# Kernel tuning notes

Hardware: AMD Instinct MI355X
Metric: run time of the kernel (lower is better)

## Reference

```python
import jax, jax.numpy as jnp
import numpy as np

TEMPERATURE = 0.1
EPS = 1e-12  # F.normalize eps


def setup_inputs() -> dict:
    key = jax.random.key(0)
    k1, k2 = jax.random.split(key)
    B, D = 4096, 128
    return {
        "x_i": jax.random.normal(k1, (B, D), dtype=jnp.float32),
        "x_j": jax.random.normal(k2, (B, D), dtype=jnp.float32),
    }


def _l2_normalize(x):
    n = jnp.sqrt(jnp.sum(x * x, axis=1, keepdims=True))
    return x / jnp.maximum(n, EPS)


def reference(x_i, x_j):
    B = x_i.shape[0]
    z = jnp.concatenate([_l2_normalize(x_i), _l2_normalize(x_j)], axis=0)  # [2B, D]
    # cosine similarity of unit-norm rows == dot product -> single GEMM
    sim = z @ z.T  # [2B, 2B]
    idx = jnp.arange(B)
    sim_ij = sim[idx, idx + B]   # diag(sim, +B)
    sim_ji = sim[idx + B, idx]   # diag(sim, -B)
    positives = jnp.concatenate([sim_ij, sim_ji], axis=0)  # [2B]
    neg_mask = 1.0 - jnp.eye(2 * B, dtype=sim.dtype)
    denominator = jnp.sum(neg_mask * jnp.exp(sim / TEMPERATURE), axis=1)  # [2B]
    # -log(exp(pos/t) / denom) = -(pos/t - log denom)
    loss_partial = jnp.log(denominator) - positives / TEMPERATURE
    return jnp.sum(loss_partial) / (2 * B)
```

## Files before the change

### kernel.cpp

```cpp
#include <hip/hip_runtime.h>
#include <stdint.h>

#define D_DIM 128
#define NROW 8192
#define L2EPS 1e-12f
#define SCALE_PRE 0.9495707f
#define LN2 0.6931471805599453f
#define NPART 50

typedef __attribute__((ext_vector_type(4))) int   i32x4;
typedef __attribute__((ext_vector_type(8))) int   i32x8;
typedef __attribute__((ext_vector_type(4))) float f32x4;

#define AS1 __attribute__((address_space(1)))
#define AS3 __attribute__((address_space(3)))

static __device__ inline void gload_lds16(const void* g, void* l) {
    __builtin_amdgcn_global_load_lds((const AS1 uint32_t*)g, (AS3 uint32_t*)l, 16, 0, 0);
}

static __device__ inline i32x8 cat8(i32x4 lo, i32x4 hi) {
    i32x8 r;
    r[0] = lo[0]; r[1] = lo[1]; r[2] = lo[2]; r[3] = lo[3];
    r[4] = hi[0]; r[5] = hi[1]; r[6] = hi[2]; r[7] = hi[3];
    return r;
}

static __device__ __forceinline__ float fexp2(float x) {
#if __has_builtin(__builtin_amdgcn_exp2f)
    return __builtin_amdgcn_exp2f(x);
#else
    float r;
    asm("v_exp_f32 %0, %1" : "=v"(r) : "v"(x));
    return r;
#endif
}

static __device__ __forceinline__ float dpp_row_sum16(float v) {
    union { float f; int i; } u, s;
    u.f = v;
    s.i = __builtin_amdgcn_update_dpp(0, u.i, 0x118, 0xF, 0xF, true); u.f += s.f;
    s.i = __builtin_amdgcn_update_dpp(0, u.i, 0x114, 0xF, 0xF, true); u.f += s.f;
    s.i = __builtin_amdgcn_update_dpp(0, u.i, 0x112, 0xF, 0xF, true); u.f += s.f;
    s.i = __builtin_amdgcn_update_dpp(0, u.i, 0x111, 0xF, 0xF, true); u.f += s.f;
    return u.f;
}

__global__ __launch_bounds__(256) void k_normalize(
        const float* __restrict__ xi, const float* __restrict__ xj,
        uint8_t* __restrict__ z8, float* __restrict__ pos_acc,
        float* __restrict__ logsum, unsigned* __restrict__ done_ct) {
    const int wave = threadIdx.x >> 6;
    const int lane = threadIdx.x & 63;
    const int row = blockIdx.x * 4 + wave;
    const float* src = (row < 4096) ? (xi + (size_t)row * D_DIM)
                                    : (xj + (size_t)(row - 4096) * D_DIM);
    float2 v = *(const float2*)(src + lane * 2);
    float ss = v.x * v.x + v.y * v.y;
#pragma unroll
    for (int m = 32; m >= 1; m >>= 1) ss += __shfl_xor(ss, m, 64);
    const float scale = SCALE_PRE / fmaxf(sqrtf(ss), L2EPS);
    const int pk = __builtin_amdgcn_cvt_pk_fp8_f32(v.x * scale, v.y * scale, 0, false);
    *(ushort*)(z8 + (size_t)row * D_DIM + lane * 2) = (ushort)pk;

    if (blockIdx.x == 0 && threadIdx.x == 0) {
        pos_acc[0] = 0.0f; logsum[0] = 0.0f; done_ct[0] = 0u;
    }
}

__global__ __launch_bounds__(256) void k_gemm(
        const uint8_t* __restrict__ z8, float* __restrict__ part,
        float* __restrict__ pos_acc) {
    __shared__ __align__(16) uint8_t lds[32768];

    const int t = threadIdx.x;
    const int wave = t >> 6, lane = t & 63;
    const int quad = lane >> 4, lc = lane & 15;

    const int mb = blockIdx.x >> 6;
    const int rb = blockIdx.x & 63;
    const int rowbase = rb * 128;
    const bool diag = (mb == 16);
    const int c1 = diag ? rb : (rb + 2 * mb + 1) & 63;
    const int c2 = (rb + 2 * mb + 2) & 63;

    {
        const uint8_t* zb1 = z8 + (size_t)c1 * 128 * D_DIM;
#pragma unroll
        for (int q = 0; q < 4; q++) {
            const int s = q * 256 + t;
            const int r = s >> 3;
            const int g = (s & 7) ^ (r & 7);
            gload_lds16(zb1 + (size_t)r * D_DIM + g * 16, &lds[s * 16]);
        }
        if (!diag) {
            const uint8_t* zb2 = z8 + (size_t)c2 * 128 * D_DIM;
#pragma unroll
            for (int q = 0; q < 4; q++) {
                const int s = q * 256 + t;
                const int r = s >> 3;
                const int g = (s & 7) ^ (r & 7);
                gload_lds16(zb2 + (size_t)r * D_DIM + g * 16, &lds[16384 + s * 16]);
            }
        }
    }

    i32x8 afr[2];
    {
        const uint8_t* pa = z8 + (size_t)(rowbase + wave * 32 + lc) * D_DIM + quad * 32;
#pragma unroll
        for (int i = 0; i < 2; i++) {
            i32x4 lo = *(const i32x4*)(pa + i * 16 * D_DIM);
            i32x4 hi = *(const i32x4*)(pa + i * 16 * D_DIM + 16);
            afr[i] = cat8(lo, hi);
        }
    }

    asm volatile("s_waitcnt vmcnt(0)" ::: "memory");
    __syncthreads();

    float rs[2][4] = {{0.f,0.f,0.f,0.f},{0.f,0.f,0.f,0.f}};
    float cs[16];
#pragma unroll
    for (int j = 0; j < 16; j++) cs[j] = 0.f;
    float posp = 0.f;
    const int rl0 = wave * 32 + quad * 4;

#define MFMA_J(j, A0, A1)                                                     \
    i32x4 blo, bhi; {                                                         \
        const int rowb = ((j) * 16 + lc) * D_DIM;                             \
        blo = *(const i32x4*)&lds[rowb + (((quad * 2)     ^ (lc & 7)) * 16)]; \
        bhi = *(const i32x4*)&lds[rowb + (((quad * 2 + 1) ^ (lc & 7)) * 16)]; \
    }                                                                         \
    const i32x8 bfr = cat8(blo, bhi);                                         \
    f32x4 z4 = {0.f, 0.f, 0.f, 0.f};                                          \
    f32x4 A0 = __builtin_amdgcn_mfma_scale_f32_16x16x128_f8f6f4(              \
                   afr[0], bfr, z4, 0, 0, 0, 131, 0, 127);                    \
    f32x4 A1 = __builtin_amdgcn_mfma_scale_f32_16x16x128_f8f6f4(              \
                   afr[1], bfr, z4, 0, 0, 0, 131, 0, 127);

    if (!diag) {
#pragma unroll
        for (int j = 0; j < 8; j++) {
            MFMA_J(j, a0, a1)
#pragma unroll
            for (int r = 0; r < 4; r++) {
                const float e0 = fexp2(a0[r]);
                const float e1 = fexp2(a1[r]);
                rs[0][r] += e0;
                rs[1][r] += e1;
                cs[j] += e0 + e1;
            }
        }
        if (mb < 15) {
#pragma unroll
            for (int j = 8; j < 16; j++) {
                MFMA_J(j, a0, a1)
#pragma unroll
                for (int r = 0; r < 4; r++) {
                    const float e0 = fexp2(a0[r]);
                    const float e1 = fexp2(a1[r]);
                    rs[0][r] += e0;
                    rs[1][r] += e1;
                    cs[j] += e0 + e1;
                }
            }
        } else {
#pragma unroll
            for (int j = 8; j < 16; j++) {
                MFMA_J(j, a0, a1)
                const int clb = (j - 8) * 16 + lc;
#pragma unroll
                for (int i = 0; i < 2; i++)
#pragma unroll
                    for (int r = 0; r < 4; r++) {
                        const float s = (i ? a1 : a0)[r];
                        const float e = 0.5f * fexp2(s);
                        if (clb == rl0 + i * 16 + r) posp += s;
                        rs[i][r] += e;
                        cs[j] += e;
                    }
            }
        }
    } else {
#pragma unroll
        for (int j = 0; j < 8; j++) {
            MFMA_J(j, a0, a1)
            const int cl = j * 16 + lc;
#pragma unroll
            for (int i = 0; i < 2; i++)
#pragma unroll
                for (int r = 0; r < 4; r++) {
                    const float s = (i ? a1 : a0)[r];
                    const float e = (cl > rl0 + i * 16 + r) ? fexp2(s) : 0.f;
                    rs[i][r] += e;
                    cs[j] += e;
                }
        }
    }
#undef MFMA_J

#pragma unroll
    for (int i = 0; i < 2; i++)
#pragma unroll
        for (int r = 0; r < 4; r++) {
            const float v = dpp_row_sum16(rs[i][r]);
            if (lc == 15)
                part[(size_t)mb * NROW + rowbase + rl0 + i * 16 + r] = v;
        }

#pragma unroll
    for (int j = 0; j < 16; j++) {
        cs[j] += __shfl_xor(cs[j], 16, 64);
        cs[j] += __shfl_xor(cs[j], 32, 64);
    }
    __syncthreads();
    float* colred = (float*)lds;
    if (quad == 0) {
#pragma unroll
        for (int j = 0; j < 16; j++)
            colred[wave * 256 + j * 16 + lc] = cs[j];
    }
    __syncthreads();
    if (t < 256) {
        const float v = colred[t] + colred[256 + t] + colred[512 + t] + colred[768 + t];
        if (!diag) {
            const int slot = 17 + 2 * mb + (t >> 7);
            const int band = (t < 128) ? c1 : c2;
            part[(size_t)slot * NROW + band * 128 + (t & 127)] = v;
        } else if (t < 128) {
            part[(size_t)49 * NROW + c1 * 128 + t] = v;
        }
    }

    if (mb == 15) {
#pragma unroll
        for (int mm = 32; mm >= 1; mm >>= 1) posp += __shfl_xor(posp, mm, 64);
        if (lane == 0) atomicAdd(pos_acc, posp);
    }
}

__global__ __launch_bounds__(256) void k_logsum(
        const float* __restrict__ part, float* __restrict__ pos_acc,
        float* __restrict__ logsum, unsigned* __restrict__ done_ct,
        float* __restrict__ out) {
    const int row = blockIdx.x * 256 + threadIdx.x;
    float d = 0.f;
#pragma unroll
    for (int p = 0; p < NPART; p++) d += part[(size_t)p * NROW + row];
    float v = __logf(d);
#pragma unroll
    for (int m = 32; m >= 1; m >>= 1) v += __shfl_xor(v, m, 64);
    if ((threadIdx.x & 63) == 0) atomicAdd(logsum, v);
    __threadfence();
    __syncthreads();
    if (threadIdx.x == 0) {
        const unsigned prev = atomicAdd(done_ct, 1u);
        if (prev == gridDim.x - 1) {
            __threadfence();
            const float ls = atomicAdd(logsum, 0.0f);
            const float pp = atomicAdd(pos_acc, 0.0f);
            out[0] = (ls - pp * LN2) / (float)NROW;
        }
    }
}

extern "C" void kernel_launch(void* const* d_in, const int* in_sizes, int n_in,
                              void* d_out, int out_size, void* d_ws, size_t ws_size,
                              hipStream_t stream) {
    const float* xi = (const float*)d_in[0];
    const float* xj = (const float*)d_in[1];
    uint8_t* z8 = (uint8_t*)d_ws;
    float* part = (float*)(z8 + (size_t)NROW * D_DIM);
    float* pos_acc = part + (size_t)NPART * NROW;
    float* logsum = pos_acc + 1;
    unsigned* done_ct = (unsigned*)(logsum + 1);
    float* out = (float*)d_out;

    hipLaunchKernelGGL(k_normalize, dim3(NROW / 4), dim3(256), 0, stream,
                       xi, xj, z8, pos_acc, logsum, done_ct);
    hipLaunchKernelGGL(k_gemm, dim3(17 * 64), dim3(256), 0, stream,
                       z8, part, pos_acc);
    hipLaunchKernelGGL(k_logsum, dim3(NROW / 256), dim3(256), 0, stream,
                       part, pos_acc, logsum, done_ct, out);
}
```

Measured before the change: 80.46 us.

## Fuse logsum reduction into GEMM kernel via last-blocks tail with atomic counter

Removes the separate k_logsum launch. The last 32 GEMM blocks to finish instead spin-wait until every block has completed, then each reduces 256 rows of partial sums, takes the log and accumulates it. A second counter picks the final block that writes the scalar output. This saves a kernel launch and its gap, but adds spin-waiting that depends on all blocks making forward progress, and the tail work now runs serially after the GEMM.

```diff
diff --git a/kernel.cpp b/kernel.cpp
--- a/kernel.cpp
+++ b/kernel.cpp
@@ -7,6 +7,8 @@
 #define SCALE_PRE 0.9495707f
 #define LN2 0.6931471805599453f
 #define NPART 50
+#define GRID (17 * 64)
+#define NTAIL 32
 
 typedef __attribute__((ext_vector_type(4))) int   i32x4;
 typedef __attribute__((ext_vector_type(8))) int   i32x8;
@@ -49,7 +51,7 @@
 __global__ __launch_bounds__(256) void k_normalize(
         const float* __restrict__ xi, const float* __restrict__ xj,
         uint8_t* __restrict__ z8, float* __restrict__ pos_acc,
-        float* __restrict__ logsum, unsigned* __restrict__ done_ct) {
+        float* __restrict__ logsum, unsigned* __restrict__ ctrs) {
     const int wave = threadIdx.x >> 6;
     const int lane = threadIdx.x & 63;
     const int row = blockIdx.x * 4 + wave;
@@ -64,13 +66,16 @@
     *(ushort*)(z8 + (size_t)row * D_DIM + lane * 2) = (ushort)pk;
 
     if (blockIdx.x == 0 && threadIdx.x == 0) {
-        pos_acc[0] = 0.0f; logsum[0] = 0.0f; done_ct[0] = 0u;
+        pos_acc[0] = 0.0f; logsum[0] = 0.0f;
+        ctrs[0] = 0u;
+        ctrs[1] = 0u;
     }
 }
 
 __global__ __launch_bounds__(256) void k_gemm(
         const uint8_t* __restrict__ z8, float* __restrict__ part,
-        float* __restrict__ pos_acc) {
+        float* __restrict__ pos_acc, float* __restrict__ logsum,
+        unsigned* __restrict__ ctrs, float* __restrict__ out) {
     __shared__ __align__(16) uint8_t lds[32768];
 
     const int t = threadIdx.x;
@@ -238,29 +243,39 @@
         for (int mm = 32; mm >= 1; mm >>= 1) posp += __shfl_xor(posp, mm, 64);
         if (lane == 0) atomicAdd(pos_acc, posp);
     }
-}
-
-__global__ __launch_bounds__(256) void k_logsum(
-        const float* __restrict__ part, float* __restrict__ pos_acc,
-        float* __restrict__ logsum, unsigned* __restrict__ done_ct,
-        float* __restrict__ out) {
-    const int row = blockIdx.x * 256 + threadIdx.x;
-    float d = 0.f;
-#pragma unroll
-    for (int p = 0; p < NPART; p++) d += part[(size_t)p * NROW + row];
-    float v = __logf(d);
-#pragma unroll
-    for (int m = 32; m >= 1; m >>= 1) v += __shfl_xor(v, m, 64);
-    if ((threadIdx.x & 63) == 0) atomicAdd(logsum, v);
-    __threadfence();
-    __syncthreads();
-    if (threadIdx.x == 0) {
-        const unsigned prev = atomicAdd(done_ct, 1u);
-        if (prev == gridDim.x - 1) {
-            __threadfence();
-            const float ls = atomicAdd(logsum, 0.0f);
-            const float pp = atomicAdd(pos_acc, 0.0f);
-            out[0] = (ls - pp * LN2) / (float)NROW;
+
+    __syncthreads();
+    if (t == 0) {
+        __threadfence();
+        ((volatile unsigned*)lds)[0] = atomicAdd(ctrs, 1u);
+    }
+    __syncthreads();
+    const unsigned prev = ((volatile unsigned*)lds)[0];
+    if (prev >= (unsigned)(GRID - NTAIL)) {
+        if (t == 0) {
+            while (__hip_atomic_load(ctrs, __ATOMIC_RELAXED,
+                                     __HIP_MEMORY_SCOPE_AGENT) < (unsigned)GRID)
+                __builtin_amdgcn_s_sleep(2);
+        }
+        __syncthreads();
+        __threadfence();
+        const int row = (int)(prev - (unsigned)(GRID - NTAIL)) * 256 + t;
+        float d = 0.f;
+#pragma unroll
+        for (int p = 0; p < NPART; p++) d += part[(size_t)p * NROW + row];
+        float v = __logf(d);
+#pragma unroll
+        for (int m = 32; m >= 1; m >>= 1) v += __shfl_xor(v, m, 64);
+        if ((t & 63) == 0) atomicAdd(logsum, v);
+        __threadfence();
+        __syncthreads();
+        if (t == 0) {
+            const unsigned p2 = atomicAdd(ctrs + 1, 1u);
+            if (p2 == (unsigned)(NTAIL - 1)) {
+                const float ls = atomicAdd(logsum, 0.0f);
+                const float pp = atomicAdd(pos_acc, 0.0f);
+                out[0] = (ls - pp * LN2) / (float)NROW;
+            }
         }
     }
 }
@@ -274,13 +289,11 @@
     float* part = (float*)(z8 + (size_t)NROW * D_DIM);
     float* pos_acc = part + (size_t)NPART * NROW;
     float* logsum = pos_acc + 1;
-    unsigned* done_ct = (unsigned*)(logsum + 1);
+    unsigned* ctrs = (unsigned*)(logsum + 1);
     float* out = (float*)d_out;
 
     hipLaunchKernelGGL(k_normalize, dim3(NROW / 4), dim3(256), 0, stream,
-                       xi, xj, z8, pos_acc, logsum, done_ct);
-    hipLaunchKernelGGL(k_gemm, dim3(17 * 64), dim3(256), 0, stream,
-                       z8, part, pos_acc);
-    hipLaunchKernelGGL(k_logsum, dim3(NROW / 256), dim3(256), 0, stream,
-                       part, pos_acc, logsum, done_ct, out);
-}
+                       xi, xj, z8, pos_acc, logsum, ctrs);
+    hipLaunchKernelGGL(k_gemm, dim3(GRID), dim3(256), 0, stream,
+                       z8, part, pos_acc, logsum, ctrs, out);
+}
```

Result: slower. 112.0 us (+39.2%).

## Load B operands directly from global memory instead of staging through LDS

Applied to the files above, without the earlier changes.

Removes the global-to-LDS staging of the two 128-row column bands. Each wave now reads its B fragments straight from global memory (L2/cache) per MFMA step. The LDS footprint shrinks to a 4 KB column-reduction buffer and launch bounds request 4 blocks per CU, which removes the initial barrier and raises occupancy. The cost is that every wave redundantly fetches the same B data through the vector memory path with uncoalesced 32-byte reads, and the memory latency is no longer hidden behind one bulk load.

```diff
diff --git a/kernel.cpp b/kernel.cpp
--- a/kernel.cpp
+++ b/kernel.cpp
@@ -11,13 +11,6 @@
 typedef __attribute__((ext_vector_type(4))) int   i32x4;
 typedef __attribute__((ext_vector_type(8))) int   i32x8;
 typedef __attribute__((ext_vector_type(4))) float f32x4;
-
-#define AS1 __attribute__((address_space(1)))
-#define AS3 __attribute__((address_space(3)))
-
-static __device__ inline void gload_lds16(const void* g, void* l) {
-    __builtin_amdgcn_global_load_lds((const AS1 uint32_t*)g, (AS3 uint32_t*)l, 16, 0, 0);
-}
 
 static __device__ inline i32x8 cat8(i32x4 lo, i32x4 hi) {
     i32x8 r;
@@ -68,10 +61,10 @@
     }
 }
 
-__global__ __launch_bounds__(256) void k_gemm(
+__global__ __launch_bounds__(256, 4) void k_gemm(
         const uint8_t* __restrict__ z8, float* __restrict__ part,
         float* __restrict__ pos_acc) {
-    __shared__ __align__(16) uint8_t lds[32768];
+    __shared__ float colred[1024];
 
     const int t = threadIdx.x;
     const int wave = t >> 6, lane = t & 63;
@@ -84,26 +77,10 @@
     const int c1 = diag ? rb : (rb + 2 * mb + 1) & 63;
     const int c2 = (rb + 2 * mb + 2) & 63;
 
-    {
-        const uint8_t* zb1 = z8 + (size_t)c1 * 128 * D_DIM;
-#pragma unroll
-        for (int q = 0; q < 4; q++) {
-            const int s = q * 256 + t;
-            const int r = s >> 3;
-            const int g = (s & 7) ^ (r & 7);
-            gload_lds16(zb1 + (size_t)r * D_DIM + g * 16, &lds[s * 16]);
-        }
-        if (!diag) {
-            const uint8_t* zb2 = z8 + (size_t)c2 * 128 * D_DIM;
-#pragma unroll
-            for (int q = 0; q < 4; q++) {
-                const int s = q * 256 + t;
-                const int r = s >> 3;
-                const int g = (s & 7) ^ (r & 7);
-                gload_lds16(zb2 + (size_t)r * D_DIM + g * 16, &lds[16384 + s * 16]);
-            }
-        }
-    }
+    const uint8_t* zb1 = z8 + (size_t)c1 * 128 * D_DIM;
+    const uint8_t* zb2 = z8 + (size_t)c2 * 128 * D_DIM;
+    const size_t boff = (size_t)lc * D_DIM + quad * 32;
+    const uint8_t* bband[2] = { zb1 + boff, (diag ? zb1 : zb2) + boff };
 
     i32x8 afr[2];
     {
@@ -116,9 +93,6 @@
         }
     }
 
-    asm volatile("s_waitcnt vmcnt(0)" ::: "memory");
-    __syncthreads();
-
     float rs[2][4] = {{0.f,0.f,0.f,0.f},{0.f,0.f,0.f,0.f}};
     float cs[16];
 #pragma unroll
@@ -128,9 +102,9 @@
 
 #define MFMA_J(j, A0, A1)                                                     \
     i32x4 blo, bhi; {                                                         \
-        const int rowb = ((j) * 16 + lc) * D_DIM;                             \
-        blo = *(const i32x4*)&lds[rowb + (((quad * 2)     ^ (lc & 7)) * 16)]; \
-        bhi = *(const i32x4*)&lds[rowb + (((quad * 2 + 1) ^ (lc & 7)) * 16)]; \
+        const uint8_t* pb = bband[(j) >> 3] + (size_t)(((j) & 7) * 16) * D_DIM; \
+        blo = *(const i32x4*)pb;                                              \
+        bhi = *(const i32x4*)(pb + 16);                                       \
     }                                                                         \
     const i32x8 bfr = cat8(blo, bhi);                                         \
     f32x4 z4 = {0.f, 0.f, 0.f, 0.f};                                          \
@@ -214,8 +188,6 @@
         cs[j] += __shfl_xor(cs[j], 16, 64);
         cs[j] += __shfl_xor(cs[j], 32, 64);
     }
-    __syncthreads();
-    float* colred = (float*)lds;
     if (quad == 0) {
 #pragma unroll
         for (int j = 0; j < 16; j++)
```

New measurement: 91.49 us. 13.7% more time.

## Enlarge off-diagonal GEMM tiles to 512x256 per block and split diagonal blocks

Applied to the files above, without the earlier changes.

Off-diagonal work is regrouped so each block computes four 128-row bands against two 128-column bands. Each wave holds a full 128-row A fragment set in registers, and five column bands (80KB) are staged in LDS. This cuts the block count from 1088 to 320 and raises operand reuse per LDS load. Diagonal blocks become a separate simplified path. The costs are much higher register and LDS pressure, lower occupancy, and fewer blocks for load balancing across CUs.

```diff
diff --git a/kernel.cpp b/kernel.cpp
--- a/kernel.cpp
+++ b/kernel.cpp
@@ -68,24 +68,153 @@
     }
 }
 
-__global__ __launch_bounds__(256) void k_gemm(
+__global__ __launch_bounds__(256, 2) void k_gemm(
         const uint8_t* __restrict__ z8, float* __restrict__ part,
         float* __restrict__ pos_acc) {
-    __shared__ __align__(16) uint8_t lds[32768];
+    __shared__ __align__(16) uint8_t lds[81920];
 
     const int t = threadIdx.x;
     const int wave = t >> 6, lane = t & 63;
     const int quad = lane >> 4, lc = lane & 15;
-
-    const int mb = blockIdx.x >> 6;
-    const int rb = blockIdx.x & 63;
+    const int bid = blockIdx.x;
+
+    if (bid < 256) {
+        const int mb = bid >> 4;
+        const int rb4 = bid & 15;
+        const int base = 4 * rb4 + 2 * mb + 1;
+
+#pragma unroll
+        for (int q = 0; q < 20; q++) {
+            const int s = q * 256 + t;
+            const int bl = s >> 10;
+            const int r = (s >> 3) & 127;
+            const int g = (s & 7) ^ (r & 7);
+            const int gb = (base + bl) & 63;
+            gload_lds16(z8 + (size_t)gb * 128 * D_DIM + (size_t)r * D_DIM + g * 16,
+                        &lds[s * 16]);
+        }
+
+        const int arow0 = (4 * rb4 + wave) * 128;
+        i32x8 afr[8];
+        {
+            const uint8_t* pa = z8 + (size_t)(arow0 + lc) * D_DIM + quad * 32;
+#pragma unroll
+            for (int i = 0; i < 8; i++) {
+                i32x4 lo = *(const i32x4*)(pa + (size_t)i * 16 * D_DIM);
+                i32x4 hi = *(const i32x4*)(pa + (size_t)i * 16 * D_DIM + 16);
+                afr[i] = cat8(lo, hi);
+            }
+        }
+
+        asm volatile("s_waitcnt vmcnt(0)" ::: "memory");
+        __syncthreads();
+
+        float rs[8][4];
+#pragma unroll
+        for (int i = 0; i < 8; i++)
+#pragma unroll
+            for (int r = 0; r < 4; r++) rs[i][r] = 0.f;
+        float cs[16];
+#pragma unroll
+        for (int j = 0; j < 16; j++) cs[j] = 0.f;
+        float posp = 0.f;
+
+#define HB_FRAG(j)                                                            \
+        i32x4 blo, bhi; {                                                     \
+            const int rowb = (wave + ((j) >> 3)) * 16384 +                    \
+                             (((j) & 7) * 16 + lc) * 128;                     \
+            blo = *(const i32x4*)&lds[rowb + (((quad * 2)     ^ (lc & 7)) * 16)]; \
+            bhi = *(const i32x4*)&lds[rowb + (((quad * 2 + 1) ^ (lc & 7)) * 16)]; \
+        }                                                                     \
+        const i32x8 bfr = cat8(blo, bhi);                                     \
+        f32x4 acc[8];                                                         \
+        {                                                                     \
+            const f32x4 z4 = {0.f, 0.f, 0.f, 0.f};                            \
+            _Pragma("unroll")                                                 \
+            for (int i = 0; i < 8; i++)                                       \
+                acc[i] = __builtin_amdgcn_mfma_scale_f32_16x16x128_f8f6f4(    \
+                             afr[i], bfr, z4, 0, 0, 0, 131, 0, 127);          \
+        }
+
+#pragma unroll
+        for (int j = 0; j < 8; j++) {
+            HB_FRAG(j)
+#pragma unroll
+            for (int i = 0; i < 8; i++)
+#pragma unroll
+                for (int r = 0; r < 4; r++) {
+                    const float e = fexp2(acc[i][r]);
+                    rs[i][r] += e;
+                    cs[j] += e;
+                }
+        }
+        if (mb < 15) {
+#pragma unroll
+            for (int j = 8; j < 16; j++) {
+                HB_FRAG(j)
+#pragma unroll
+                for (int i = 0; i < 8; i++)
+#pragma unroll
+                    for (int r = 0; r < 4; r++) {
+                        const float e = fexp2(acc[i][r]);
+                        rs[i][r] += e;
+                        cs[j] += e;
+                    }
+            }
+        } else {
+#pragma unroll
+            for (int j = 8; j < 16; j++) {
+                HB_FRAG(j)
+#pragma unroll
+                for (int i = 0; i < 8; i++)
+#pragma unroll
+                    for (int r = 0; r < 4; r++) {
+                        const float s = acc[i][r];
+                        const float e = 0.5f * fexp2(s);
+                        if (((j & 7) == i) && (lc == quad * 4 + r)) posp += s;
+                        rs[i][r] += e;
+                        cs[j] += e;
+                    }
+            }
+        }
+#undef HB_FRAG
+
+#pragma unroll
+        for (int i = 0; i < 8; i++)
+#pragma unroll
+            for (int r = 0; r < 4; r++) {
+                const float v = dpp_row_sum16(rs[i][r]);
+                if (lc == 15)
+                    part[(size_t)mb * NROW + arow0 + i * 16 + quad * 4 + r] = v;
+            }
+
+#pragma unroll
+        for (int j = 0; j < 16; j++) {
+            cs[j] += __shfl_xor(cs[j], 16, 64);
+            cs[j] += __shfl_xor(cs[j], 32, 64);
+        }
+        if (quad == 0) {
+#pragma unroll
+            for (int j = 0; j < 16; j++) {
+                const int gb = (base + wave + (j >> 3)) & 63;
+                const int slot = 17 + 2 * mb + (j >> 3);
+                part[(size_t)slot * NROW + gb * 128 + (j & 7) * 16 + lc] = cs[j];
+            }
+        }
+
+        if (mb == 15) {
+#pragma unroll
+            for (int mm = 32; mm >= 1; mm >>= 1) posp += __shfl_xor(posp, mm, 64);
+            if (lane == 0) atomicAdd(pos_acc, posp);
+        }
+        return;
+    }
+
+    const int rb = bid - 256;
     const int rowbase = rb * 128;
-    const bool diag = (mb == 16);
-    const int c1 = diag ? rb : (rb + 2 * mb + 1) & 63;
-    const int c2 = (rb + 2 * mb + 2) & 63;
 
     {
-        const uint8_t* zb1 = z8 + (size_t)c1 * 128 * D_DIM;
+        const uint8_t* zb1 = z8 + (size_t)rb * 128 * D_DIM;
 #pragma unroll
         for (int q = 0; q < 4; q++) {
             const int s = q * 256 + t;
@@ -93,16 +222,6 @@
             const int g = (s & 7) ^ (r & 7);
             gload_lds16(zb1 + (size_t)r * D_DIM + g * 16, &lds[s * 16]);
         }
-        if (!diag) {
-            const uint8_t* zb2 = z8 + (size_t)c2 * 128 * D_DIM;
-#pragma unroll
-            for (int q = 0; q < 4; q++) {
-                const int s = q * 256 + t;
-                const int r = s >> 3;
-                const int g = (s & 7) ^ (r & 7);
-                gload_lds16(zb2 + (size_t)r * D_DIM + g * 16, &lds[16384 + s * 16]);
-            }
-        }
     }
 
     i32x8 afr[2];
@@ -123,82 +242,32 @@
     float cs[16];
 #pragma unroll
     for (int j = 0; j < 16; j++) cs[j] = 0.f;
-    float posp = 0.f;
     const int rl0 = wave * 32 + quad * 4;
 
-#define MFMA_J(j, A0, A1)                                                     \
-    i32x4 blo, bhi; {                                                         \
-        const int rowb = ((j) * 16 + lc) * D_DIM;                             \
-        blo = *(const i32x4*)&lds[rowb + (((quad * 2)     ^ (lc & 7)) * 16)]; \
-        bhi = *(const i32x4*)&lds[rowb + (((quad * 2 + 1) ^ (lc & 7)) * 16)]; \
-    }                                                                         \
-    const i32x8 bfr = cat8(blo, bhi);                                         \
-    f32x4 z4 = {0.f, 0.f, 0.f, 0.f};                                          \
-    f32x4 A0 = __builtin_amdgcn_mfma_scale_f32_16x16x128_f8f6f4(              \
-                   afr[0], bfr, z4, 0, 0, 0, 131, 0, 127);                    \
-    f32x4 A1 = __builtin_amdgcn_mfma_scale_f32_16x16x128_f8f6f4(              \
-                   afr[1], bfr, z4, 0, 0, 0, 131, 0, 127);
-
-    if (!diag) {
-#pragma unroll
-        for (int j = 0; j < 8; j++) {
-            MFMA_J(j, a0, a1)
+#pragma unroll
+    for (int j = 0; j < 8; j++) {
+        i32x4 blo, bhi; {
+            const int rowb = (j * 16 + lc) * D_DIM;
+            blo = *(const i32x4*)&lds[rowb + (((quad * 2)     ^ (lc & 7)) * 16)];
+            bhi = *(const i32x4*)&lds[rowb + (((quad * 2 + 1) ^ (lc & 7)) * 16)];
+        }
+        const i32x8 bfr = cat8(blo, bhi);
+        const f32x4 z4 = {0.f, 0.f, 0.f, 0.f};
+        f32x4 a0 = __builtin_amdgcn_mfma_scale_f32_16x16x128_f8f6f4(
+                       afr[0], bfr, z4, 0, 0, 0, 131, 0, 127);
+        f32x4 a1 = __builtin_amdgcn_mfma_scale_f32_16x16x128_f8f6f4(
+                       afr[1], bfr, z4, 0, 0, 0, 131, 0, 127);
+        const int cl = j * 16 + lc;
+#pragma unroll
+        for (int i = 0; i < 2; i++)
 #pragma unroll
             for (int r = 0; r < 4; r++) {
-                const float e0 = fexp2(a0[r]);
-                const float e1 = fexp2(a1[r]);
-                rs[0][r] += e0;
-                rs[1][r] += e1;
-                cs[j] += e0 + e1;
-            }
-        }
-        if (mb < 15) {
-#pragma unroll
-            for (int j = 8; j < 16; j++) {
-                MFMA_J(j, a0, a1)
-#pragma unroll
-                for (int r = 0; r < 4; r++) {
-                    const float e0 = fexp2(a0[r]);
-                    const float e1 = fexp2(a1[r]);
-                    rs[0][r] += e0;
-                    rs[1][r] += e1;
-                    cs[j] += e0 + e1;
-                }
-            }
-        } else {
-#pragma unroll
-            for (int j = 8; j < 16; j++) {
-                MFMA_J(j, a0, a1)
-                const int clb = (j - 8) * 16 + lc;
-#pragma unroll
-                for (int i = 0; i < 2; i++)
-#pragma unroll
-                    for (int r = 0; r < 4; r++) {
-                        const float s = (i ? a1 : a0)[r];
-                        const float e = 0.5f * fexp2(s);
-                        if (clb == rl0 + i * 16 + r) posp += s;
-                        rs[i][r] += e;
-                        cs[j] += e;
-                    }
-            }
-        }
-    } else {
-#pragma unroll
-        for (int j = 0; j < 8; j++) {
-            MFMA_J(j, a0, a1)
-            const int cl = j * 16 + lc;
-#pragma unroll
-            for (int i = 0; i < 2; i++)
-#pragma unroll
-                for (int r = 0; r < 4; r++) {
-                    const float s = (i ? a1 : a0)[r];
-                    const float e = (cl > rl0 + i * 16 + r) ? fexp2(s) : 0.f;
-                    rs[i][r] += e;
-                    cs[j] += e;
-                }
-        }
-    }
-#undef MFMA_J
+                const float s = (i ? a1 : a0)[r];
+                const float e = (cl > rl0 + i * 16 + r) ? fexp2(s) : 0.f;
+                rs[i][r] += e;
+                cs[j] += e;
+            }
+    }
 
 #pragma unroll
     for (int i = 0; i < 2; i++)
@@ -206,7 +275,7 @@
         for (int r = 0; r < 4; r++) {
             const float v = dpp_row_sum16(rs[i][r]);
             if (lc == 15)
-                part[(size_t)mb * NROW + rowbase + rl0 + i * 16 + r] = v;
+                part[(size_t)16 * NROW + rowbase + rl0 + i * 16 + r] = v;
         }
 
 #pragma unroll
@@ -222,21 +291,9 @@
             colred[wave * 256 + j * 16 + lc] = cs[j];
     }
     __syncthreads();
-    if (t < 256) {
+    if (t < 128) {
         const float v = colred[t] + colred[256 + t] + colred[512 + t] + colred[768 + t];
-        if (!diag) {
-            const int slot = 17 + 2 * mb + (t >> 7);
-            const int band = (t < 128) ? c1 : c2;
-            part[(size_t)slot * NROW + band * 128 + (t & 127)] = v;
-        } else if (t < 128) {
-            part[(size_t)49 * NROW + c1 * 128 + t] = v;
-        }
-    }
-
-    if (mb == 15) {
-#pragma unroll
-        for (int mm = 32; mm >= 1; mm >>= 1) posp += __shfl_xor(posp, mm, 64);
-        if (lane == 0) atomicAdd(pos_acc, posp);
+        part[(size_t)49 * NROW + rb * 128 + t] = v;
     }
 }
 
@@ -279,7 +336,7 @@
 
     hipLaunchKernelGGL(k_normalize, dim3(NROW / 4), dim3(256), 0, stream,
                        xi, xj, z8, pos_acc, logsum, done_ct);
-    hipLaunchKernelGGL(k_gemm, dim3(17 * 64), dim3(256), 0, stream,
+    hipLaunchKernelGGL(k_gemm, dim3(256 + 64), dim3(256), 0, stream,
                        z8, part, pos_acc);
     hipLaunchKernelGGL(k_logsum, dim3(NROW / 256), dim3(256), 0, stream,
                        part, pos_acc, logsum, done_ct, out);
```

Result: slower. 95.22 us (+18.4%).
